# Performance work log

Hardware: AMD Instinct MI355X
Metric: run time of the kernel (lower is better)

## Reference

```python
import jax, jax.numpy as jnp
import numpy as np

B, N, EG = 4, 16384, 131072
H, DK, DV, DM = 4, 32, 32, 128


def setup_inputs() -> dict:
    key = jax.random.key(0)
    ks = jax.random.split(key, 12)
    s = 0.05
    return {
        "edge_indices": jax.random.randint(ks[0], (B, 2, EG), 0, N, dtype=jnp.int32),
        "edge_features": jax.random.normal(ks[1], (B, EG, DM), jnp.float32),
        "input_Q": jax.random.normal(ks[2], (B, N, DM), jnp.float32),
        "input_K": jax.random.normal(ks[3], (B, N, DM), jnp.float32),
        "input_V": jax.random.normal(ks[4], (B, N, DM), jnp.float32),
        "W_Q": jax.random.normal(ks[5], (DM, H * DK), jnp.float32) * s,
        "W_K": jax.random.normal(ks[6], (DM, H * DK), jnp.float32) * s,
        "W_V": jax.random.normal(ks[7], (DM, H * DV), jnp.float32) * s,
        "W_E": jax.random.normal(ks[8], (DM, H * DV), jnp.float32) * s,
        "W_fc": jax.random.normal(ks[9], (H * DV, DM), jnp.float32) * s,
        "ln_gamma": jnp.ones((DM,), jnp.float32),
        "ln_beta": jnp.zeros((DM,), jnp.float32),
    }


def _layer_norm(x, g, b, eps=1e-5):
    mu = jnp.mean(x, axis=-1, keepdims=True)
    var = jnp.mean(jnp.square(x - mu), axis=-1, keepdims=True)
    return g * (x - mu) * jax.lax.rsqrt(var + eps) + b


def _proj(x, W, d):
    # [B, T, DM] @ [DM, H*d] -> [B, H, T, d]
    bsz, t, _ = x.shape
    return (x @ W).reshape(bsz, t, H, d).transpose(0, 2, 1, 3)


def reference(edge_indices, edge_features, input_Q, input_K, input_V,
              W_Q, W_K, W_V, W_E, W_fc, ln_gamma, ln_beta):
    residual = input_Q
    bsz, n_nodes, _ = input_Q.shape
    Q = _proj(input_Q, W_Q, DK)        # [B,H,N,dk]
    K = _proj(input_K, W_K, DK)
    V = _proj(input_V, W_V, DV)
    E = _proj(edge_features, W_E, DV)  # [B,H,Eg,dv]

    inv_sqrt_dk = 1.0 / np.sqrt(DK).astype(np.float32)

    def one_graph(Qb, Kb, Vb, Eb, idx):
        src, tgt = idx[0], idx[1]                       # [Eg]
        Qe = Qb[:, src]                                  # [H,Eg,dk]
        Ke = Kb[:, tgt]
        Ve = Vb[:, tgt]
        scores = (Qe * Ke) * inv_sqrt_dk * Eb            # [H,Eg,dv]
        attn = jnp.exp(jnp.clip(scores.sum(-1, keepdims=True), -5.0, 5.0))  # [H,Eg,1]
        msg = attn * Ve                                  # [H,Eg,dv]
        num = jnp.zeros((H, n_nodes, DV), Qb.dtype).at[:, src].add(msg)
        den = jnp.zeros((H, n_nodes, 1), Qb.dtype).at[:, src].add(attn)
        return num / (den + 1e-8), attn

    out, attn = jax.vmap(one_graph)(Q, K, V, E, edge_indices)  # [B,H,N,dv], [B,H,Eg,1]

    out = out.transpose(0, 2, 1, 3).reshape(bsz, n_nodes, H * DV)
    out = out @ W_fc
    out = _layer_norm(out + residual, ln_gamma, ln_beta)
    # torch code returns attn from the last batch iteration (leading dim 1)
    return out, attn[-1:]
```

## Files before the change

### kernel.cpp

```cpp
#include <hip/hip_runtime.h>

#define BB 4
#define NN 16384
#define EGc 131072
#define CAP 64
#define INVSQ 0.17677669529663687f

typedef unsigned int uint;
typedef unsigned short ushort;
typedef short short8 __attribute__((ext_vector_type(8)));
typedef float floatx4 __attribute__((ext_vector_type(4)));

__device__ __forceinline__ float bflo(uint u) { return __uint_as_float(u << 16); }
__device__ __forceinline__ float bfhi(uint u) { return __uint_as_float(u & 0xffff0000u); }
__device__ __forceinline__ ushort f2bf(float f) {
    uint u = __float_as_uint(f);
    u += 0x7fffu + ((u >> 16) & 1u);
    return (ushort)(u >> 16);
}

#define SA_STRIDE 136
#define SW_STRIDE 136
#define SY_STRIDE 132
struct __align__(16) SMem {
    union {
        struct {
            ushort sA[64 * SA_STRIDE];
            ushort sW[128 * SW_STRIDE];
        };
        float  sY[64 * SY_STRIDE];
        ushort sOut[64 * 128];
    };
};

__device__ __forceinline__ void stage_x(SMem& sm, const float4* __restrict__ X4,
                                        size_t r0, int t) {
#pragma unroll
    for (int i = 0; i < 8; ++i) {
        int f = t + 256 * i;
        int r = f >> 5, c4 = f & 31;
        float4 x = X4[(r0 + r) * 32 + c4];
        ushort4 h;
        h.x = f2bf(x.x); h.y = f2bf(x.y); h.z = f2bf(x.z); h.w = f2bf(x.w);
        *(ushort4*)&sm.sA[r * SA_STRIDE + c4 * 4] = h;
    }
}

__device__ __forceinline__ void stage_wt(SMem& sm, const uint4* __restrict__ Wt4, int t) {
#pragma unroll
    for (int i = 0; i < 8; ++i) {
        int f = t + 256 * i;
        int c = f >> 4, kc = f & 15;
        uint4 w = Wt4[f];
        *(uint4*)&sm.sW[c * SW_STRIDE + kc * 8] = w;
    }
}

__device__ __forceinline__ void mfma_core(const SMem& sm, int t, floatx4 (&acc)[2][4]) {
    int lane = t & 63, w = t >> 6;
    int wr = (w >> 1) * 32, wc = (w & 1) * 64;
    int m = lane & 15, q = lane >> 4;
#pragma unroll
    for (int ks = 0; ks < 4; ++ks) {
        int k = ks * 32 + q * 8;
        short8 a0 = *(const short8*)&sm.sA[(wr + m) * SA_STRIDE + k];
        short8 a1 = *(const short8*)&sm.sA[(wr + 16 + m) * SA_STRIDE + k];
#pragma unroll
        for (int j = 0; j < 4; ++j) {
            short8 b = *(const short8*)&sm.sW[(wc + j * 16 + m) * SW_STRIDE + k];
            acc[0][j] = __builtin_amdgcn_mfma_f32_16x16x32_bf16(a0, b, acc[0][j], 0, 0, 0);
            acc[1][j] = __builtin_amdgcn_mfma_f32_16x16x32_bf16(a1, b, acc[1][j], 0, 0, 0);
        }
    }
}

__device__ __forceinline__ void acc_zero(floatx4 (&acc)[2][4]) {
    floatx4 z = {0.f, 0.f, 0.f, 0.f};
#pragma unroll
    for (int i = 0; i < 2; ++i)
#pragma unroll
        for (int j = 0; j < 4; ++j) acc[i][j] = z;
}

__device__ __forceinline__ void acc_to_sy(SMem& sm, int t, const floatx4 (&acc)[2][4]) {
    int lane = t & 63, w = t >> 6;
    int wr = (w >> 1) * 32, wc = (w & 1) * 64;
    int m = lane & 15, q = lane >> 4;
#pragma unroll
    for (int i = 0; i < 2; ++i)
#pragma unroll
        for (int j = 0; j < 4; ++j)
#pragma unroll
            for (int r = 0; r < 4; ++r)
                sm.sY[(wr + i * 16 + q * 4 + r) * SY_STRIDE + wc + j * 16 + m] = acc[i][j][r];
}

__global__ __launch_bounds__(256) void transpose_w(const float* __restrict__ W0,
                                                   const float* __restrict__ W1,
                                                   const float* __restrict__ W2,
                                                   const float* __restrict__ W3,
                                                   const float* __restrict__ W4,
                                                   ushort* __restrict__ Wt) {
    __shared__ ushort sT[128 * 136];
    int bi = blockIdx.x;
    const float* W = bi == 0 ? W0 : bi == 1 ? W1 : bi == 2 ? W2 : bi == 3 ? W3 : W4;
    int t = threadIdx.x;
    const float4* Wp = (const float4*)W;
#pragma unroll
    for (int i = 0; i < 16; ++i) {
        int f = t + 256 * i;
        int d = f >> 5, c4 = f & 31;
        float4 w = Wp[f];
        sT[(c4 * 4 + 0) * 136 + d] = f2bf(w.x);
        sT[(c4 * 4 + 1) * 136 + d] = f2bf(w.y);
        sT[(c4 * 4 + 2) * 136 + d] = f2bf(w.z);
        sT[(c4 * 4 + 3) * 136 + d] = f2bf(w.w);
    }
    __syncthreads();
    uint4* out = (uint4*)(Wt + (size_t)bi * 16384);
#pragma unroll
    for (int i = 0; i < 8; ++i) {
        int f = t + 256 * i;
        int c = f >> 4, kc = f & 15;
        out[f] = *(const uint4*)&sT[c * 136 + kc * 8];
    }
}

__global__ __launch_bounds__(256) void proj_mfma(const float* __restrict__ IQ,
                                                 const float* __restrict__ IK,
                                                 const float* __restrict__ IV,
                                                 const ushort* __restrict__ WtAll,
                                                 ushort* __restrict__ Qp,
                                                 ushort* __restrict__ Kp,
                                                 ushort* __restrict__ Vp) {
    __shared__ SMem sm;
    int t = threadIdx.x;
    const float* X; const ushort* Wt; ushort* Y;
    if (blockIdx.y == 0)      { X = IQ; Wt = WtAll;         Y = Qp; }
    else if (blockIdx.y == 1) { X = IK; Wt = WtAll + 16384; Y = Kp; }
    else                      { X = IV; Wt = WtAll + 32768; Y = Vp; }
    size_t r0 = (size_t)blockIdx.x * 64;
    stage_x(sm, (const float4*)X, r0, t);
    stage_wt(sm, (const uint4*)Wt, t);
    __syncthreads();
    floatx4 acc[2][4];
    acc_zero(acc);
    mfma_core(sm, t, acc);
    __syncthreads();
    {
        int lane = t & 63, w = t >> 6;
        int wr = (w >> 1) * 32, wc = (w & 1) * 64;
        int m = lane & 15, q = lane >> 4;
#pragma unroll
        for (int i = 0; i < 2; ++i)
#pragma unroll
            for (int j = 0; j < 4; ++j)
#pragma unroll
                for (int r = 0; r < 4; ++r)
                    sm.sOut[(wr + i * 16 + q * 4 + r) * 128 + wc + j * 16 + m] = f2bf(acc[i][j][r]);
    }
    __syncthreads();
    uint4* Y4 = (uint4*)Y;
#pragma unroll
    for (int i = 0; i < 4; ++i) {
        int f = t + 256 * i;
        Y4[r0 * 16 + f] = *(const uint4*)&sm.sOut[f * 8];
    }
}

__global__ __launch_bounds__(256, 3) void edge_kernel(const int* __restrict__ EI,
                                                      const float* __restrict__ EF,
                                                      const ushort* __restrict__ WtE,
                                                      const ushort* __restrict__ Qp,
                                                      const ushort* __restrict__ Kp,
                                                      float* __restrict__ aArr,
                                                      int* __restrict__ list,
                                                      int* __restrict__ cnt,
                                                      float* __restrict__ attn_out) {
    __shared__ SMem sm;
    int t = threadIdx.x;
    int b = blockIdx.x >> 11;
    int tile = blockIdx.x & 2047;
    int e0 = tile * 64;
    int w = t >> 6, lane = t & 63;

    if (t < 64) {
        int ge = e0 + t;
        int src = EI[(size_t)b * 2 * EGc + ge];
        int tgt = EI[(size_t)b * 2 * EGc + EGc + ge];
        int slot = atomicAdd(&cnt[b * NN + src], 1);
        if (slot < CAP) list[((size_t)(b * NN + src)) * CAP + slot] = (tgt << 17) | ge;
    }

    int e16 = w * 16 + (lane & 15);
    int srcv = EI[(size_t)b * 2 * EGc + e0 + e16];
    int tgtv = EI[(size_t)b * 2 * EGc + EGc + e0 + e16];
    const uint* Qu = (const uint*)Qp;
    const uint* Ku = (const uint*)Kp;
    uint q01[16], k01[16];
#pragma unroll
    for (int ei = 0; ei < 16; ++ei) {
        int s = __shfl(srcv, ei, 16);
        int g = __shfl(tgtv, ei, 16);
        q01[ei] = Qu[((size_t)b * NN + s) * 64 + lane];
        k01[ei] = Ku[((size_t)b * NN + g) * 64 + lane];
    }

    stage_x(sm, (const float4*)EF, (size_t)b * EGc + e0, t);
    stage_wt(sm, (const uint4*)WtE, t);
    __syncthreads();
    floatx4 acc[2][4];
    acc_zero(acc);
    mfma_core(sm, t, acc);
    __syncthreads();
    acc_to_sy(sm, t, acc);
    __syncthreads();

    int h = lane >> 4;
    bool isLast = (b == BB - 1);
#pragma unroll
    for (int ei = 0; ei < 16; ++ei) {
        int e = w * 16 + ei;
        float2 ev = *(const float2*)&sm.sY[e * SY_STRIDE + 2 * lane];
        float p = bflo(q01[ei]) * bflo(k01[ei]) * ev.x + bfhi(q01[ei]) * bfhi(k01[ei]) * ev.y;
        p += __shfl_xor(p, 8, 64);
        p += __shfl_xor(p, 4, 64);
        p += __shfl_xor(p, 2, 64);
        p += __shfl_xor(p, 1, 64);
        float av = __expf(fminf(fmaxf(p * INVSQ, -5.f), 5.f));
        int ge = e0 + e;
        if ((lane & 15) == 0) {
            aArr[((size_t)b * EGc + ge) * 4 + h] = av;
            if (isLast) attn_out[(size_t)h * EGc + ge] = av;
        }
    }
}

__global__ __launch_bounds__(256) void finalize_kernel(const ushort* __restrict__ Vp,
                                                       const float* __restrict__ aArr,
                                                       const int* __restrict__ list,
                                                       const int* __restrict__ cnt,
                                                       const ushort* __restrict__ WtFC,
                                                       const float* __restrict__ IQ,
                                                       const float* __restrict__ G,
                                                       const float* __restrict__ Bt,
                                                       float* __restrict__ Out) {
    __shared__ SMem sm;
    int t = threadIdx.x;
    size_t r0 = (size_t)blockIdx.x * 64;
    int b = (int)(r0 >> 14);
    stage_wt(sm, (const uint4*)WtFC, t);

    int w = t >> 6, lane = t & 63;
    int h = lane >> 4;
    const uint* Vu = (const uint*)Vp;
    const float* aBase = aArr + (size_t)b * EGc * 4;

    for (int ni = 0; ni < 16; ++ni) {
        int row = w * 16 + ni;
        size_t grow = r0 + row;
        int deg = cnt[grow];
        deg = deg < CAP ? deg : CAP;
        int le = 0, tv = 0;
        if (lane < deg) {
            int pk = list[grow * CAP + lane];
            le = pk & 0x1FFFF;
            tv = pk >> 17;
        }
        float afp0, afp1 = 0.f, afp2 = 0.f, afp3 = 0.f;
        {
            int m0 = __shfl(le, lane & 15, 64);
            afp0 = aBase[(size_t)m0 * 4 + h];
            if (deg > 16) { int m1 = __shfl(le, 16 + (lane & 15), 64); afp1 = aBase[(size_t)m1 * 4 + h]; }
            if (deg > 32) { int m2 = __shfl(le, 32 + (lane & 15), 64); afp2 = aBase[(size_t)m2 * 4 + h]; }
            if (deg > 48) { int m3 = __shfl(le, 48 + (lane & 15), 64); afp3 = aBase[(size_t)m3 * 4 + h]; }
        }
        float n0 = 0.f, n1 = 0.f, dh = 0.f;
#define FCHUNK(K, AFP) \
        if (deg > 16 * K) { \
            int lim = deg - 16 * K; lim = lim > 16 ? 16 : lim; \
            _Pragma("unroll 8") \
            for (int j2 = 0; j2 < lim; ++j2) { \
                int tgt = __shfl(tv, 16 * K + j2, 64); \
                float af = __shfl(AFP, (lane & 48) + j2, 64); \
                uint v01 = Vu[((size_t)b * NN + tgt) * 64 + lane]; \
                n0 += af * bflo(v01); n1 += af * bfhi(v01); dh += af; \
            } \
        }
        FCHUNK(0, afp0)
        FCHUNK(1, afp1)
        FCHUNK(2, afp2)
        FCHUNK(3, afp3)
#undef FCHUNK
        float inv = 1.f / (dh + 1e-8f);
        uint packed = (uint)f2bf(n0 * inv) | ((uint)f2bf(n1 * inv) << 16);
        *(uint*)&sm.sA[row * SA_STRIDE + 2 * lane] = packed;
    }
    __syncthreads();
    floatx4 acc[2][4];
    acc_zero(acc);
    mfma_core(sm, t, acc);
    __syncthreads();
    acc_to_sy(sm, t, acc);
    __syncthreads();

    float g0 = G[lane], g1 = G[lane + 64];
    float be0 = Bt[lane], be1 = Bt[lane + 64];
    for (int ei = 0; ei < 16; ++ei) {
        int e = w * 16 + ei;
        size_t row = r0 + e;
        float y0 = sm.sY[e * SY_STRIDE + lane]      + IQ[row * 128 + lane];
        float y1 = sm.sY[e * SY_STRIDE + lane + 64] + IQ[row * 128 + lane + 64];
        float s = y0 + y1;
        float qq = y0 * y0 + y1 * y1;
#pragma unroll
        for (int off = 32; off >= 1; off >>= 1) {
            s  += __shfl_xor(s, off, 64);
            qq += __shfl_xor(qq, off, 64);
        }
        float mu = s * (1.f / 128.f);
        float var = qq * (1.f / 128.f) - mu * mu;
        float rstd = rsqrtf(var + 1e-5f);
        Out[row * 128 + lane]      = g0 * (y0 - mu) * rstd + be0;
        Out[row * 128 + lane + 64] = g1 * (y1 - mu) * rstd + be1;
    }
}

extern "C" void kernel_launch(void* const* d_in, const int* in_sizes, int n_in,
                              void* d_out, int out_size, void* d_ws, size_t ws_size,
                              hipStream_t stream) {
    const int*   EI  = (const int*)d_in[0];
    const float* EF  = (const float*)d_in[1];
    const float* IQ  = (const float*)d_in[2];
    const float* IK  = (const float*)d_in[3];
    const float* IV  = (const float*)d_in[4];
    const float* WQ  = (const float*)d_in[5];
    const float* WK  = (const float*)d_in[6];
    const float* WV  = (const float*)d_in[7];
    const float* WE  = (const float*)d_in[8];
    const float* WFC = (const float*)d_in[9];
    const float* G   = (const float*)d_in[10];
    const float* Bt  = (const float*)d_in[11];

    char* ws = (char*)d_ws;
    ushort* Qp   = (ushort*)ws;
    ushort* Kp   = (ushort*)(ws + 16777216);
    ushort* Vp   = (ushort*)(ws + 2 * 16777216);
    ushort* Wt   = (ushort*)(ws + 3 * 16777216);
    float*  aArr = (float*) (ws + 3 * 16777216 + 262144);
    int*    list = (int*)   (ws + 3 * 16777216 + 262144 + 8388608);
    int*    cnt  = (int*)   (ws + 4 * 16777216 + 262144 + 8388608);

    float* out0 = (float*)d_out;
    float* attn_out = out0 + (size_t)BB * NN * 128;

    hipMemsetAsync(cnt, 0, (size_t)BB * NN * sizeof(int), stream);

    transpose_w<<<5, 256, 0, stream>>>(WQ, WK, WV, WE, WFC, Wt);

    dim3 pg(1024, 3);
    proj_mfma<<<pg, 256, 0, stream>>>(IQ, IK, IV, Wt, Qp, Kp, Vp);

    edge_kernel<<<BB * (EGc / 64), 256, 0, stream>>>(EI, EF, Wt + 3 * 16384,
                                                     Qp, Kp, aArr, list, cnt, attn_out);

    finalize_kernel<<<1024, 256, 0, stream>>>(Vp, aArr, list, cnt,
                                              Wt + 4 * 16384, IQ, G, Bt, out0);
}
```

Measured before the change: 665.5 us.

## Split finalize into high-occupancy gather kernel and separate FC+LayerNorm kernel

The fused finalize kernel, which did the per-node neighbour gather and then the FC matmul plus LayerNorm, is split into two kernels. The gather kernel launches four times as many blocks, gives each wave 4 nodes instead of 16, uses no shared memory, and writes bf16 aggregated rows to a global buffer that reuses the Q projection buffer. A second kernel loads those rows into shared memory and runs the MFMA FC and LayerNorm. The aim is more memory-level parallelism and occupancy for the latency-bound gather, at the cost of an extra global round trip and an extra launch.

```diff
diff --git a/kernel.cpp b/kernel.cpp
--- a/kernel.cpp
+++ b/kernel.cpp
@@ -236,30 +236,26 @@
     }
 }
 
-__global__ __launch_bounds__(256) void finalize_kernel(const ushort* __restrict__ Vp,
-                                                       const float* __restrict__ aArr,
-                                                       const int* __restrict__ list,
-                                                       const int* __restrict__ cnt,
-                                                       const ushort* __restrict__ WtFC,
-                                                       const float* __restrict__ IQ,
-                                                       const float* __restrict__ G,
-                                                       const float* __restrict__ Bt,
-                                                       float* __restrict__ Out) {
-    __shared__ SMem sm;
-    int t = threadIdx.x;
-    size_t r0 = (size_t)blockIdx.x * 64;
-    int b = (int)(r0 >> 14);
-    stage_wt(sm, (const uint4*)WtFC, t);
-
+__global__ __launch_bounds__(256) void gather_kernel(const ushort* __restrict__ Vp,
+                                                     const float* __restrict__ aArr,
+                                                     const int* __restrict__ list,
+                                                     const int* __restrict__ cnt,
+                                                     uint* __restrict__ Xg) {
+    int t = threadIdx.x;
     int w = t >> 6, lane = t & 63;
+    int wid = blockIdx.x * 4 + w;
+    size_t n0 = (size_t)wid * 4;
+    int b = (int)(n0 >> 14);
     int h = lane >> 4;
     const uint* Vu = (const uint*)Vp;
     const float* aBase = aArr + (size_t)b * EGc * 4;
 
-    for (int ni = 0; ni < 16; ++ni) {
-        int row = w * 16 + ni;
-        size_t grow = r0 + row;
-        int deg = cnt[grow];
+    int degv = 0;
+    if (lane < 4) degv = cnt[n0 + lane];
+
+    for (int ni = 0; ni < 4; ++ni) {
+        size_t grow = n0 + ni;
+        int deg = __shfl(degv, ni, 64);
         deg = deg < CAP ? deg : CAP;
         int le = 0, tv = 0;
         if (lane < deg) {
@@ -275,7 +271,7 @@
             if (deg > 32) { int m2 = __shfl(le, 32 + (lane & 15), 64); afp2 = aBase[(size_t)m2 * 4 + h]; }
             if (deg > 48) { int m3 = __shfl(le, 48 + (lane & 15), 64); afp3 = aBase[(size_t)m3 * 4 + h]; }
         }
-        float n0 = 0.f, n1 = 0.f, dh = 0.f;
+        float n0v = 0.f, n1v = 0.f, dh = 0.f;
 #define FCHUNK(K, AFP) \
         if (deg > 16 * K) { \
             int lim = deg - 16 * K; lim = lim > 16 ? 16 : lim; \
@@ -284,7 +280,7 @@
                 int tgt = __shfl(tv, 16 * K + j2, 64); \
                 float af = __shfl(AFP, (lane & 48) + j2, 64); \
                 uint v01 = Vu[((size_t)b * NN + tgt) * 64 + lane]; \
-                n0 += af * bflo(v01); n1 += af * bfhi(v01); dh += af; \
+                n0v += af * bflo(v01); n1v += af * bfhi(v01); dh += af; \
             } \
         }
         FCHUNK(0, afp0)
@@ -293,9 +289,29 @@
         FCHUNK(3, afp3)
 #undef FCHUNK
         float inv = 1.f / (dh + 1e-8f);
-        uint packed = (uint)f2bf(n0 * inv) | ((uint)f2bf(n1 * inv) << 16);
-        *(uint*)&sm.sA[row * SA_STRIDE + 2 * lane] = packed;
-    }
+        uint packed = (uint)f2bf(n0v * inv) | ((uint)f2bf(n1v * inv) << 16);
+        Xg[grow * 64 + lane] = packed;
+    }
+}
+
+__global__ __launch_bounds__(256) void fc_ln_kernel(const uint* __restrict__ Xg,
+                                                    const ushort* __restrict__ WtFC,
+                                                    const float* __restrict__ IQ,
+                                                    const float* __restrict__ G,
+                                                    const float* __restrict__ Bt,
+                                                    float* __restrict__ Out) {
+    __shared__ SMem sm;
+    int t = threadIdx.x;
+    size_t r0 = (size_t)blockIdx.x * 64;
+    const uint4* X4 = (const uint4*)(Xg + r0 * 64);
+#pragma unroll
+    for (int i = 0; i < 4; ++i) {
+        int f = t + 256 * i;
+        int r = f >> 4, c = f & 15;
+        uint4 x = X4[f];
+        *(uint4*)&sm.sA[r * SA_STRIDE + c * 8] = x;
+    }
+    stage_wt(sm, (const uint4*)WtFC, t);
     __syncthreads();
     floatx4 acc[2][4];
     acc_zero(acc);
@@ -304,6 +320,7 @@
     acc_to_sy(sm, t, acc);
     __syncthreads();
 
+    int w = t >> 6, lane = t & 63;
     float g0 = G[lane], g1 = G[lane + 64];
     float be0 = Bt[lane], be1 = Bt[lane + 64];
     for (int ei = 0; ei < 16; ++ei) {
@@ -364,6 +381,8 @@
     edge_kernel<<<BB * (EGc / 64), 256, 0, stream>>>(EI, EF, Wt + 3 * 16384,
                                                      Qp, Kp, aArr, list, cnt, attn_out);
 
-    finalize_kernel<<<1024, 256, 0, stream>>>(Vp, aArr, list, cnt,
-                                              Wt + 4 * 16384, IQ, G, Bt, out0);
-}
+    uint* Xg = (uint*)Qp;
+    gather_kernel<<<4096, 256, 0, stream>>>(Vp, aArr, list, cnt, Xg);
+
+    fc_ln_kernel<<<1024, 256, 0, stream>>>(Xg, Wt + 4 * 16384, IQ, G, Bt, out0);
+}
```

Result: faster. 574.0 us (-13.7%).
